# Optimization experiments

Hardware: AMD Instinct MI355X
Metric: run time of the kernel (lower is better)

Reference implementation:

```python
import jax, jax.numpy as jnp
import numpy as np

M1, N1, M2, N2 = 32, 64, 24, 48  # Kronecker block dims; 32*24=768, 64*48=3072


def setup_inputs() -> dict:
    key = jax.random.key(0)
    k1, k2, k3, k4, k5 = jax.random.split(key, 5)
    rank = 64
    x = jax.random.normal(k1, (4, 4096, 768), dtype=jnp.float32)
    A_factors = jax.random.normal(k2, (M1 * N1, rank), dtype=jnp.float32) * 0.05
    B_factors = jax.random.normal(k3, (rank, M2 * N2), dtype=jnp.float32) * 0.05
    # 'Sparse' residual is materialized dense in the original module (to_dense()).
    Sparse = jax.random.normal(k4, (768, 3072), dtype=jnp.float32) * 0.02
    bias = jax.random.normal(k5, (3072,), dtype=jnp.float32) * 0.02
    return {"x": x, "A_factors": A_factors, "B_factors": B_factors,
            "Sparse": Sparse, "bias": bias}


def reference(x, A_factors, B_factors, Sparse, bias):
    # Low-rank product: [2048, r] @ [r, 1152] -> [2048, 1152]
    W_tilde = A_factors @ B_factors
    # Kronecker permute: (m1, n1, m2, n2) -> (m1, m2, n1, n2) -> [768, 3072]
    W_low = W_tilde.reshape(M1, N1, M2, N2).transpose(0, 2, 1, 3).reshape(
        M1 * M2, N1 * N2)
    W = W_low + Sparse
    # Dense GEMM: [B, S, 768] @ [768, 3072] + bias
    return x @ W + bias
```

## Files before the change

kernel.cpp:

```cpp
#include <hip/hip_runtime.h>
#include <hip/hip_bf16.h>
#include <stdint.h>

#define M_TOT 16384
#define N_TOT 3072
#define K_TOT 768

#define BM 256
#define BN 128
#define BK 32
#define NT (K_TOT / BK)

typedef __attribute__((ext_vector_type(8))) short short8;
typedef __attribute__((ext_vector_type(4))) float f32x4;

__device__ __forceinline__ unsigned short f2bf(float f) {
    union { float f; unsigned u; } v;
    v.f = f;
    unsigned r = v.u + 0x7FFFu + ((v.u >> 16) & 1u);
    return (unsigned short)(r >> 16);
}

__global__ __launch_bounds__(384) void prep_cvt_kernel(
    const float* __restrict__ Af, const float* __restrict__ Bf,
    const float* __restrict__ Sp, const float* __restrict__ x,
    unsigned short* __restrict__ xb, unsigned short* __restrict__ Wt) {
    __shared__ float a_sh[4][64];
    __shared__ float wrow[4][1160];
    const int tid = threadIdx.x;
    const int b = blockIdx.x;

    if (b < 512) {
        const int m1 = b >> 4;
        const int n10 = (b & 15) * 4;
        if (tid < 256) {
            int rr = tid >> 6, k = tid & 63;
            a_sh[rr][k] = Af[(size_t)(m1 * 64 + n10 + rr) * 64 + k];
        }
        __syncthreads();
        float acc[4][3] = {};
        #pragma unroll 2
        for (int k = 0; k < 64; ++k) {
            const float* brow = Bf + (size_t)k * 1152;
            float b0 = brow[tid], b1 = brow[tid + 384], b2 = brow[tid + 768];
            #pragma unroll
            for (int rr = 0; rr < 4; ++rr) {
                float a = a_sh[rr][k];
                acc[rr][0] = fmaf(a, b0, acc[rr][0]);
                acc[rr][1] = fmaf(a, b1, acc[rr][1]);
                acc[rr][2] = fmaf(a, b2, acc[rr][2]);
            }
        }
        #pragma unroll
        for (int rr = 0; rr < 4; ++rr) {
            wrow[rr][tid] = acc[rr][0];
            wrow[rr][tid + 384] = acc[rr][1];
            wrow[rr][tid + 768] = acc[rr][2];
        }
        __syncthreads();
        if (tid < 192) {
            const int rr = tid / 48, n2 = tid % 48;
            const int c = (n10 + rr) * 48 + n2;
            const int r0 = m1 * 24;
            unsigned w[12];
            #pragma unroll
            for (int t2 = 0; t2 < 12; ++t2) {
                float lo = wrow[rr][(2 * t2) * 48 + n2]
                         + Sp[(size_t)(r0 + 2 * t2) * 3072 + c];
                float hi = wrow[rr][(2 * t2 + 1) * 48 + n2]
                         + Sp[(size_t)(r0 + 2 * t2 + 1) * 3072 + c];
                w[t2] = (unsigned)f2bf(lo) | ((unsigned)f2bf(hi) << 16);
            }
            uint4* d4 = reinterpret_cast<uint4*>(Wt + (size_t)c * 768 + r0);
            d4[0] = (uint4){w[0], w[1], w[2], w[3]};
            d4[1] = (uint4){w[4], w[5], w[6], w[7]};
            d4[2] = (uint4){w[8], w[9], w[10], w[11]};
        }
    } else {
        const int n8 = M_TOT * K_TOT / 8;
        int i = (b - 512) * 384 + tid;
        const int stride = 2048 * 384;
        const float4* xv = reinterpret_cast<const float4*>(x);
        uint4* ov = reinterpret_cast<uint4*>(xb);
        for (; i < n8; i += stride) {
            float4 a = xv[2 * i], c = xv[2 * i + 1];
            uint4 o;
            o.x = (unsigned)f2bf(a.x) | ((unsigned)f2bf(a.y) << 16);
            o.y = (unsigned)f2bf(a.z) | ((unsigned)f2bf(a.w) << 16);
            o.z = (unsigned)f2bf(c.x) | ((unsigned)f2bf(c.y) << 16);
            o.w = (unsigned)f2bf(c.z) | ((unsigned)f2bf(c.w) << 16);
            ov[i] = o;
        }
    }
}

__device__ __forceinline__ void gld16(const void* g, void* l) {
    __builtin_amdgcn_global_load_lds(
        (const __attribute__((address_space(1))) void*)g,
        (__attribute__((address_space(3))) void*)l, 16, 0, 0);
}

__global__ __launch_bounds__(256, 2) void gemm_bt_kernel(
    const unsigned short* __restrict__ A, const unsigned short* __restrict__ Bt,
    const float* __restrict__ bias, float* __restrict__ C) {
    __shared__ unsigned short As[3][BM * BK];
    __shared__ unsigned short Bs[3][BN * BK];

    const int tid = threadIdx.x;
    const int lane = tid & 63;
    const int wid = tid >> 6;
    const int wr = wid >> 1;
    const int wc = wid & 1;

    const int xcd = blockIdx.x & 7, g = blockIdx.x >> 3;
    const int c = g >> 6, h = g & 63;
    const int bm = xcd * 8 + (h >> 3);
    const int bn = c * 8 + (h & 7);
    const int brow = bm * BM, bcol = bn * BN;

    const int srow = tid >> 2;
    const int soff = (((tid & 3) ^ ((tid >> 3) & 3)) << 4);
    const char* pA = (const char*)A + ((size_t)(brow + srow) * K_TOT) * 2 + soff;
    const char* pB = (const char*)Bt + ((size_t)(bcol + srow) * K_TOT) * 2 + soff;
    const size_t rstep = (size_t)64 * K_TOT * 2;
    const int tid16 = tid * 16;

#define STG(bu, t) do {                                                          \
        const char* sa_ = pA + (size_t)(t) * (BK * 2);                           \
        const char* sb_ = pB + (size_t)(t) * (BK * 2);                           \
        gld16(sa_,             (char*)&As[bu][0] + tid16);                       \
        gld16(sa_ + rstep,     (char*)&As[bu][0] + tid16 + 4096);                \
        gld16(sa_ + 2 * rstep, (char*)&As[bu][0] + tid16 + 8192);                \
        gld16(sa_ + 3 * rstep, (char*)&As[bu][0] + tid16 + 12288);               \
        gld16(sb_,             (char*)&Bs[bu][0] + tid16);                       \
        gld16(sb_ + rstep,     (char*)&Bs[bu][0] + tid16 + 4096); } while (0)

    const int la = lane & 15;
    const int g4 = lane >> 4;
    const int swb = ((g4 ^ ((lane >> 1) & 3)) << 4);
#define FRAG_A(bu, r) (*(const short8*)((const char*)&As[bu][0] + (r) * 64 + swb))
#define FRAG_B(bu, r) (*(const short8*)((const char*)&Bs[bu][0] + (r) * 64 + swb))

    f32x4 acc[8][4];
    #pragma unroll
    for (int m = 0; m < 8; ++m)
        #pragma unroll
        for (int n = 0; n < 4; ++n)
            acc[m][n] = (f32x4){0.f, 0.f, 0.f, 0.f};

    STG(0, 0); STG(1, 1);
    asm volatile("s_waitcnt vmcnt(6)" ::: "memory");
    __builtin_amdgcn_s_barrier();
    __builtin_amdgcn_sched_barrier(0);

    const int arow = wr * 128;
    const int bcolw = wc * 64;

    #pragma unroll 1
    for (int t = 0; t < NT; ++t) {
        const int bu = t % 3;
        short8 a_[4], b_[4];

        if (t + 2 < NT) STG((t + 2) % 3, t + 2);
        #pragma unroll
        for (int n = 0; n < 4; ++n) b_[n] = FRAG_B(bu, bcolw + n * 16 + la);
        #pragma unroll
        for (int m = 0; m < 4; ++m) a_[m] = FRAG_A(bu, arow + m * 16 + la);
        __builtin_amdgcn_s_setprio(1);
        #pragma unroll
        for (int m = 0; m < 4; ++m)
            #pragma unroll
            for (int n = 0; n < 4; ++n)
                acc[m][n] = __builtin_amdgcn_mfma_f32_16x16x32_bf16(
                    b_[n], a_[m], acc[m][n], 0, 0, 0);
        __builtin_amdgcn_s_setprio(0);

        #pragma unroll
        for (int m = 0; m < 4; ++m) a_[m] = FRAG_A(bu, arow + 64 + m * 16 + la);
        __builtin_amdgcn_s_setprio(1);
        #pragma unroll
        for (int m = 0; m < 4; ++m)
            #pragma unroll
            for (int n = 0; n < 4; ++n)
                acc[4 + m][n] = __builtin_amdgcn_mfma_f32_16x16x32_bf16(
                    b_[n], a_[m], acc[4 + m][n], 0, 0, 0);
        __builtin_amdgcn_s_setprio(0);

        if (t < NT - 1) {
            if (t + 2 < NT) asm volatile("s_waitcnt vmcnt(6)" ::: "memory");
            else            asm volatile("s_waitcnt vmcnt(0)" ::: "memory");
            __builtin_amdgcn_s_barrier();
            __builtin_amdgcn_sched_barrier(0);
        }
    }

    #pragma unroll
    for (int n = 0; n < 4; ++n) {
        const int gc = bcol + bcolw + n * 16 + g4 * 4;
        const f32x4 bv = *reinterpret_cast<const f32x4*>(&bias[gc]);
        #pragma unroll
        for (int m = 0; m < 8; ++m) {
            const int gr = brow + arow + m * 16 + la;
            f32x4 o = {acc[m][n][0] + bv[0], acc[m][n][1] + bv[1],
                       acc[m][n][2] + bv[2], acc[m][n][3] + bv[3]};
            *reinterpret_cast<f32x4*>(&C[(size_t)gr * N_TOT + gc]) = o;
        }
    }
#undef STG
#undef FRAG_A
#undef FRAG_B
}

extern "C" void kernel_launch(void* const* d_in, const int* in_sizes, int n_in,
                              void* d_out, int out_size, void* d_ws, size_t ws_size,
                              hipStream_t stream) {
    const float* x    = (const float*)d_in[0];
    const float* Af   = (const float*)d_in[1];
    const float* Bf   = (const float*)d_in[2];
    const float* Sp   = (const float*)d_in[3];
    const float* bias = (const float*)d_in[4];
    float* out = (float*)d_out;

    unsigned short* xb = (unsigned short*)d_ws;
    unsigned short* wt = xb + (size_t)M_TOT * K_TOT;

    hipLaunchKernelGGL(prep_cvt_kernel, dim3(512 + 2048), dim3(384), 0, stream,
                       Af, Bf, Sp, x, xb, wt);
    hipLaunchKernelGGL(gemm_bt_kernel,
                       dim3((M_TOT / BM) * (N_TOT / BN)), dim3(256),
                       0, stream, xb, wt, bias, out);
}
```

Measured before the change: 139.3 us.

## Replace triple-buffered 256x128 GEMM with single-buffered 128x128 BK64 tiles

Shrinks the GEMM block tile from 256x128 to 128x128 and doubles the K step to 64. It drops the triple-buffered async prefetch pipeline in favour of a simple load-barrier-compute loop on a single LDS buffer. It also uses a new 8-slot XOR swizzle and a linear XCD-strided block mapping, and raises the occupancy hint to 3 blocks per CU. The aim is to hide memory latency through more resident blocks and smaller per-block state rather than in-block prefetching. The cost is that loads no longer overlap compute within a block, A and B tiles are reused less, and the loop has two barriers per iteration.

```diff
diff --git a/kernel.cpp b/kernel.cpp
--- a/kernel.cpp
+++ b/kernel.cpp
@@ -6,9 +6,9 @@
 #define N_TOT 3072
 #define K_TOT 768
 
-#define BM 256
+#define BM 128
 #define BN 128
-#define BK 32
+#define BK 64
 #define NT (K_TOT / BK)
 
 typedef __attribute__((ext_vector_type(8))) short short8;
@@ -100,11 +100,11 @@
         (__attribute__((address_space(3))) void*)l, 16, 0, 0);
 }
 
-__global__ __launch_bounds__(256, 2) void gemm_bt_kernel(
+__global__ __launch_bounds__(256, 3) void gemm_bt_kernel(
     const unsigned short* __restrict__ A, const unsigned short* __restrict__ Bt,
     const float* __restrict__ bias, float* __restrict__ C) {
-    __shared__ unsigned short As[3][BM * BK];
-    __shared__ unsigned short Bs[3][BN * BK];
+    __shared__ unsigned short As[BM * BK];
+    __shared__ unsigned short Bs[BN * BK];
 
     const int tid = threadIdx.x;
     const int lane = tid & 63;
@@ -112,85 +112,63 @@
     const int wr = wid >> 1;
     const int wc = wid & 1;
 
-    const int xcd = blockIdx.x & 7, g = blockIdx.x >> 3;
-    const int c = g >> 6, h = g & 63;
-    const int bm = xcd * 8 + (h >> 3);
-    const int bn = c * 8 + (h & 7);
+    const int wg = (blockIdx.x & 7) * 384 + (blockIdx.x >> 3);
+    const int bm = wg / (N_TOT / BN), bn = wg % (N_TOT / BN);
     const int brow = bm * BM, bcol = bn * BN;
 
-    const int srow = tid >> 2;
-    const int soff = (((tid & 3) ^ ((tid >> 3) & 3)) << 4);
-    const char* pA = (const char*)A + ((size_t)(brow + srow) * K_TOT) * 2 + soff;
-    const char* pB = (const char*)Bt + ((size_t)(bcol + srow) * K_TOT) * 2 + soff;
-    const size_t rstep = (size_t)64 * K_TOT * 2;
+    const int srow = tid >> 3;
+    const int sslot = (tid & 7) ^ ((tid >> 3) & 7);
+    const char* pA = (const char*)A + ((size_t)(brow + srow) * K_TOT + sslot * 8) * 2;
+    const char* pB = (const char*)Bt + ((size_t)(bcol + srow) * K_TOT + sslot * 8) * 2;
+    const size_t rstep = (size_t)32 * K_TOT * 2;
     const int tid16 = tid * 16;
 
-#define STG(bu, t) do {                                                          \
-        const char* sa_ = pA + (size_t)(t) * (BK * 2);                           \
-        const char* sb_ = pB + (size_t)(t) * (BK * 2);                           \
-        gld16(sa_,             (char*)&As[bu][0] + tid16);                       \
-        gld16(sa_ + rstep,     (char*)&As[bu][0] + tid16 + 4096);                \
-        gld16(sa_ + 2 * rstep, (char*)&As[bu][0] + tid16 + 8192);                \
-        gld16(sa_ + 3 * rstep, (char*)&As[bu][0] + tid16 + 12288);               \
-        gld16(sb_,             (char*)&Bs[bu][0] + tid16);                       \
-        gld16(sb_ + rstep,     (char*)&Bs[bu][0] + tid16 + 4096); } while (0)
+#define STG(t) do {                                                              \
+        _Pragma("unroll")                                                        \
+        for (int r_ = 0; r_ < 4; ++r_)                                           \
+            gld16(pA + r_ * rstep + (size_t)(t) * 128,                           \
+                  (char*)As + r_ * 4096 + tid16);                                \
+        _Pragma("unroll")                                                        \
+        for (int r_ = 0; r_ < 4; ++r_)                                           \
+            gld16(pB + r_ * rstep + (size_t)(t) * 128,                           \
+                  (char*)Bs + r_ * 4096 + tid16); } while (0)
 
     const int la = lane & 15;
     const int g4 = lane >> 4;
-    const int swb = ((g4 ^ ((lane >> 1) & 3)) << 4);
-#define FRAG_A(bu, r) (*(const short8*)((const char*)&As[bu][0] + (r) * 64 + swb))
-#define FRAG_B(bu, r) (*(const short8*)((const char*)&Bs[bu][0] + (r) * 64 + swb))
-
-    f32x4 acc[8][4];
+#define FRAG(base, row, s) (*(const short8*)((const char*)(base) +               \
+        (row) * 128 + (((s) ^ ((row) & 7)) << 4)))
+
+    f32x4 acc[4][4];
     #pragma unroll
-    for (int m = 0; m < 8; ++m)
+    for (int m = 0; m < 4; ++m)
         #pragma unroll
         for (int n = 0; n < 4; ++n)
             acc[m][n] = (f32x4){0.f, 0.f, 0.f, 0.f};
 
-    STG(0, 0); STG(1, 1);
-    asm volatile("s_waitcnt vmcnt(6)" ::: "memory");
-    __builtin_amdgcn_s_barrier();
-    __builtin_amdgcn_sched_barrier(0);
-
-    const int arow = wr * 128;
+    const int arow = wr * 64;
     const int bcolw = wc * 64;
 
     #pragma unroll 1
     for (int t = 0; t < NT; ++t) {
-        const int bu = t % 3;
-        short8 a_[4], b_[4];
-
-        if (t + 2 < NT) STG((t + 2) % 3, t + 2);
-        #pragma unroll
-        for (int n = 0; n < 4; ++n) b_[n] = FRAG_B(bu, bcolw + n * 16 + la);
-        #pragma unroll
-        for (int m = 0; m < 4; ++m) a_[m] = FRAG_A(bu, arow + m * 16 + la);
-        __builtin_amdgcn_s_setprio(1);
-        #pragma unroll
-        for (int m = 0; m < 4; ++m)
-            #pragma unroll
-            for (int n = 0; n < 4; ++n)
-                acc[m][n] = __builtin_amdgcn_mfma_f32_16x16x32_bf16(
-                    b_[n], a_[m], acc[m][n], 0, 0, 0);
-        __builtin_amdgcn_s_setprio(0);
-
-        #pragma unroll
-        for (int m = 0; m < 4; ++m) a_[m] = FRAG_A(bu, arow + 64 + m * 16 + la);
-        __builtin_amdgcn_s_setprio(1);
-        #pragma unroll
-        for (int m = 0; m < 4; ++m)
-            #pragma unroll
-            for (int n = 0; n < 4; ++n)
-                acc[4 + m][n] = __builtin_amdgcn_mfma_f32_16x16x32_bf16(
-                    b_[n], a_[m], acc[4 + m][n], 0, 0, 0);
-        __builtin_amdgcn_s_setprio(0);
-
-        if (t < NT - 1) {
-            if (t + 2 < NT) asm volatile("s_waitcnt vmcnt(6)" ::: "memory");
-            else            asm volatile("s_waitcnt vmcnt(0)" ::: "memory");
-            __builtin_amdgcn_s_barrier();
-            __builtin_amdgcn_sched_barrier(0);
+        __syncthreads();
+        STG(t);
+        __syncthreads();
+        #pragma unroll
+        for (int kk = 0; kk < 2; ++kk) {
+            const int s = kk * 4 + g4;
+            short8 af[4], bf_[4];
+            #pragma unroll
+            for (int n = 0; n < 4; ++n) bf_[n] = FRAG(Bs, bcolw + n * 16 + la, s);
+            #pragma unroll
+            for (int m = 0; m < 4; ++m) af[m] = FRAG(As, arow + m * 16 + la, s);
+            __builtin_amdgcn_s_setprio(1);
+            #pragma unroll
+            for (int m = 0; m < 4; ++m)
+                #pragma unroll
+                for (int n = 0; n < 4; ++n)
+                    acc[m][n] = __builtin_amdgcn_mfma_f32_16x16x32_bf16(
+                        bf_[n], af[m], acc[m][n], 0, 0, 0);
+            __builtin_amdgcn_s_setprio(0);
         }
     }
 
@@ -199,7 +177,7 @@
         const int gc = bcol + bcolw + n * 16 + g4 * 4;
         const f32x4 bv = *reinterpret_cast<const f32x4*>(&bias[gc]);
         #pragma unroll
-        for (int m = 0; m < 8; ++m) {
+        for (int m = 0; m < 4; ++m) {
             const int gr = brow + arow + m * 16 + la;
             f32x4 o = {acc[m][n][0] + bv[0], acc[m][n][1] + bv[1],
                        acc[m][n][2] + bv[2], acc[m][n][3] + bv[3]};
@@ -207,8 +185,7 @@
         }
     }
 #undef STG
-#undef FRAG_A
-#undef FRAG_B
+#undef FRAG
 }
 
 extern "C" void kernel_launch(void* const* d_in, const int* in_sizes, int n_in,
```

Result: faster. 127.2 us (-8.7%).
